# Kernel optimization log

Measured on AMD Instinct MI355X. Metric: run time of the kernel, lower is better.

The kernel has to match this reference:

```python
import jax, jax.numpy as jnp
import numpy as np

OUT_F, IN_F = 4096, 4096
NNZ = 838860
TOKENS = (8, 2048)


def setup_inputs() -> dict:
    key = jax.random.key(0)
    k1, k2, k3, k4, k5 = jax.random.split(key, 5)
    inp = {
        "input": jax.random.normal(k1, (*TOKENS, IN_F), dtype=jnp.float32),
        "dense_weights": jax.random.normal(k2, (OUT_F, IN_F), dtype=jnp.float32) * 0.02,
        "dense_bias": jax.random.normal(k3, (OUT_F,), dtype=jnp.float32) * 0.02,
        "sparse_weights": jax.random.normal(k4, (NNZ,), dtype=jnp.float32) * 0.02,
        "nz_idx": jnp.sort(jax.random.randint(k5, (NNZ,), 0, OUT_F * IN_F, dtype=jnp.int32)),
    }
    return inp


def reference(input, dense_weights, dense_bias, sparse_weights, nz_idx):
    # csr_add: scatter sparse delta into dense weight (CSR expressed as sorted flat indices)
    out_f, in_f = dense_weights.shape
    rows = nz_idx // in_f
    cols = nz_idx % in_f
    weights = dense_weights.at[rows, cols].add(sparse_weights)  # [out_f, in_f]
    # F.linear: x @ W.T + b
    return jnp.einsum('bsi,oi->bso', input, weights) + dense_bias
```

## Files before the change

### kernel.cpp

```cpp
#include <hip/hip_runtime.h>

typedef __bf16 bf16x8 __attribute__((ext_vector_type(8)));
typedef float  f32x4  __attribute__((ext_vector_type(4)));

#define IN_F  4096
#define OUT_F 4096
#define BM 256
#define BN 256
#define BK 32
#define NBUF 4
#define TILE_ELEMS (BM * BK)

__device__ inline unsigned int pk_bf16(float a, float b) {
  unsigned int ua = __float_as_uint(a);
  unsigned int ub = __float_as_uint(b);
  ua = (ua + 0x7FFFu + ((ua >> 16) & 1u)) >> 16;
  ub = (ub + 0x7FFFu + ((ub >> 16) & 1u)) >> 16;
  return ua | (ub << 16);
}
__device__ inline unsigned short bf16_1(float a) {
  unsigned int u = __float_as_uint(a);
  return (unsigned short)((u + 0x7FFFu + ((u >> 16) & 1u)) >> 16);
}

__global__ void cvt_f32_bf16_x8(const float4* __restrict__ src, uint4* __restrict__ dst, int n8) {
  int i = blockIdx.x * 256 + threadIdx.x;
  if (i >= n8) return;
  float4 a = src[2 * i];
  float4 b = src[2 * i + 1];
  uint4 o;
  o.x = pk_bf16(a.x, a.y);
  o.y = pk_bf16(a.z, a.w);
  o.z = pk_bf16(b.x, b.y);
  o.w = pk_bf16(b.z, b.w);
  dst[i] = o;
}

__global__ void sparse_fix_k(const float* __restrict__ dw, const int* __restrict__ idx,
                             const float* __restrict__ sv, unsigned short* __restrict__ wb,
                             int nnz) {
  int i = blockIdx.x * 256 + threadIdx.x;
  if (i >= nnz) return;
  int id = idx[i];
  if (i > 0 && idx[i - 1] == id) return;
  float s = sv[i];
  int j = i + 1;
  while (j < nnz && idx[j] == id) { s += sv[j]; ++j; }
  wb[id] = bf16_1(dw[id] + s);
}

__global__ __launch_bounds__(512, 2) void gemm256(
    const unsigned short* __restrict__ Xb,
    const unsigned short* __restrict__ Wb,
    const float* __restrict__ bias,
    float* __restrict__ out,
    int M, int N, int K)
{
  __shared__ __align__(16) unsigned short lA[NBUF * TILE_ELEMS];
  __shared__ __align__(16) unsigned short lB[NBUF * TILE_ELEMS];

  const int t    = threadIdx.x;
  const int w    = t >> 6;
  const int lane = t & 63;
  const int quad = lane >> 4;
  const int l16  = lane & 15;
  const int wr   = w >> 2;
  const int wc   = w & 3;

  const int nwg = gridDim.x;
  const int cpx = nwg >> 3;
  const int sid = (blockIdx.x & 7) * cpx + (blockIdx.x >> 3);
  const int gn  = N / BN;
  const int tile_n = (sid % gn) * BN;
  const int tile_m = (sid / gn) * BM;

  const int c0 = t, c1 = 512 + t;
  const int r0 = c0 >> 2, r1 = c1 >> 2;
  const int s0 = ((c0 & 3) ^ ((r0 >> 1) & 3)) * 8;
  const int s1 = ((c1 & 3) ^ ((r1 >> 1) & 3)) * 8;
  const unsigned short* aS0 = Xb + (size_t)(tile_m + r0) * K + s0;
  const unsigned short* aS1 = Xb + (size_t)(tile_m + r1) * K + s1;
  const unsigned short* bS0 = Wb + (size_t)(tile_n + r0) * K + s0;
  const unsigned short* bS1 = Wb + (size_t)(tile_n + r1) * K + s1;

#define GLD(src, dst) __builtin_amdgcn_global_load_lds( \
      (const __attribute__((address_space(1))) unsigned int*)(src), \
      (__attribute__((address_space(3))) unsigned int*)(dst), 16, 0, 0)
#define STAGE_A(tt) do { const int _b = ((tt) & 3) * TILE_ELEMS; const int _kb = (tt) * BK; \
      GLD(aS0 + _kb, lA + _b + c0 * 8); GLD(aS1 + _kb, lA + _b + c1 * 8); } while (0)
#define STAGE_B(tt) do { const int _b = ((tt) & 3) * TILE_ELEMS; const int _kb = (tt) * BK; \
      GLD(bS0 + _kb, lB + _b + c0 * 8); GLD(bS1 + _kb, lB + _b + c1 * 8); } while (0)

  int offA[8], offB[4];
#pragma unroll
  for (int mi = 0; mi < 8; ++mi) {
    const int ra = wr * 128 + mi * 16 + l16;
    offA[mi] = ra * BK + (quad ^ ((ra >> 1) & 3)) * 8;
  }
#pragma unroll
  for (int ni = 0; ni < 4; ++ni) {
    const int rb = wc * 64 + ni * 16 + l16;
    offB[ni] = rb * BK + (quad ^ ((rb >> 1) & 3)) * 8;
  }

  f32x4 acc[8][4] = {};
  const int nt = K / BK;

  STAGE_A(0); STAGE_B(0);
  STAGE_A(1); STAGE_B(1);
  STAGE_A(2); STAGE_B(2);
  asm volatile("s_waitcnt vmcnt(8)" ::: "memory");
  __builtin_amdgcn_s_barrier();

  for (int tt = 0; tt < nt; ++tt) {
    const unsigned short* bufA = lA + (tt & 3) * TILE_ELEMS;
    const unsigned short* bufB = lB + (tt & 3) * TILE_ELEMS;

    bf16x8 af0[4], bfr[4];
#pragma unroll
    for (int mi = 0; mi < 4; ++mi) af0[mi] = *(const bf16x8*)&bufA[offA[mi]];
#pragma unroll
    for (int ni = 0; ni < 4; ++ni) bfr[ni] = *(const bf16x8*)&bufB[offB[ni]];
    if (tt + 3 < nt) STAGE_A(tt + 3);
    __builtin_amdgcn_s_barrier();
    __builtin_amdgcn_s_setprio(1);
#pragma unroll
    for (int mi = 0; mi < 4; ++mi)
#pragma unroll
      for (int ni = 0; ni < 4; ++ni)
        acc[mi][ni] = __builtin_amdgcn_mfma_f32_16x16x32_bf16(af0[mi], bfr[ni], acc[mi][ni], 0, 0, 0);
    __builtin_amdgcn_s_setprio(0);
    __builtin_amdgcn_s_barrier();

    bf16x8 af1[4];
#pragma unroll
    for (int mi = 0; mi < 4; ++mi) af1[mi] = *(const bf16x8*)&bufA[offA[4 + mi]];
    if (tt + 3 < nt) STAGE_B(tt + 3);
    if (tt < nt - 3)       asm volatile("s_waitcnt vmcnt(8)" ::: "memory");
    else if (tt == nt - 3) asm volatile("s_waitcnt vmcnt(4)" ::: "memory");
    else if (tt == nt - 2) asm volatile("s_waitcnt vmcnt(0)" ::: "memory");
    __builtin_amdgcn_s_barrier();
    __builtin_amdgcn_s_setprio(1);
#pragma unroll
    for (int mi = 0; mi < 4; ++mi)
#pragma unroll
      for (int ni = 0; ni < 4; ++ni)
        acc[4 + mi][ni] = __builtin_amdgcn_mfma_f32_16x16x32_bf16(af1[mi], bfr[ni], acc[4 + mi][ni], 0, 0, 0);
    __builtin_amdgcn_s_setprio(0);
    __builtin_amdgcn_s_barrier();
  }

#pragma unroll
  for (int ni = 0; ni < 4; ++ni) {
    const int n = tile_n + wc * 64 + ni * 16 + l16;
    const float bv = bias[n];
#pragma unroll
    for (int mi = 0; mi < 8; ++mi) {
      const int m0 = tile_m + wr * 128 + mi * 16 + quad * 4;
#pragma unroll
      for (int r = 0; r < 4; ++r)
        out[(size_t)(m0 + r) * N + n] = acc[mi][ni][r] + bv;
    }
  }
#undef GLD
#undef STAGE_A
#undef STAGE_B
}

extern "C" void kernel_launch(void* const* d_in, const int* in_sizes, int n_in,
                              void* d_out, int out_size, void* d_ws, size_t ws_size,
                              hipStream_t stream) {
  const float* x    = (const float*)d_in[0];
  const float* dw   = (const float*)d_in[1];
  const float* bias = (const float*)d_in[2];
  const float* sv   = (const float*)d_in[3];
  const int*   idx  = (const int*)d_in[4];
  float* out = (float*)d_out;

  const int K = IN_F, N = OUT_F;
  const int M   = in_sizes[0] / K;
  const int nnz = in_sizes[3];
  const int WN  = N * K;

  unsigned short* ws_xb = (unsigned short*)d_ws;
  unsigned short* ws_wb = (unsigned short*)((char*)d_ws + (size_t)in_sizes[0] * 2);

  cvt_f32_bf16_x8<<<WN / 8 / 256, 256, 0, stream>>>((const float4*)dw, (uint4*)ws_wb, WN / 8);
  sparse_fix_k<<<(nnz + 255) / 256, 256, 0, stream>>>(dw, idx, sv, ws_wb, nnz);
  const int xn = in_sizes[0];
  cvt_f32_bf16_x8<<<xn / 8 / 256, 256, 0, stream>>>((const float4*)x, (uint4*)ws_xb, xn / 8);
  const int nblocks = (M / BM) * (N / BN);
  gemm256<<<nblocks, 512, 0, stream>>>(ws_xb, ws_wb, bias, out, M, N, K);
}
```

Before: 1.067 ms.

## Restructure GEMM mainloop to BK=64 double-buffered half-tile staging pipeline

Replaces the 4-buffer BK=32 ring with two BK=64 buffers, each split into two 32-wide halves. Every iteration now runs four MFMA phases, and the global-to-LDS loads for the next halves are staged between phases, with a separate peeled epilogue for the last tile. The aim is fewer loop iterations and finer-grained overlap of loads with compute while keeping the same LDS footprint. The wait and barrier counts are hand-tuned, so an ordering mistake could cause stalls or races.

```diff
diff --git a/kernel.cpp b/kernel.cpp
--- a/kernel.cpp
+++ b/kernel.cpp
@@ -7,8 +7,8 @@
 #define OUT_F 4096
 #define BM 256
 #define BN 256
-#define BK 32
-#define NBUF 4
+#define BK 64
+#define HALF_ELEMS (BM * 32)
 #define TILE_ELEMS (BM * BK)
 
 __device__ inline unsigned int pk_bf16(float a, float b) {
@@ -56,8 +56,8 @@
     float* __restrict__ out,
     int M, int N, int K)
 {
-  __shared__ __align__(16) unsigned short lA[NBUF * TILE_ELEMS];
-  __shared__ __align__(16) unsigned short lB[NBUF * TILE_ELEMS];
+  __shared__ __align__(16) unsigned short lA[2 * TILE_ELEMS];
+  __shared__ __align__(16) unsigned short lB[2 * TILE_ELEMS];
 
   const int t    = threadIdx.x;
   const int w    = t >> 6;
@@ -78,76 +78,143 @@
   const int r0 = c0 >> 2, r1 = c1 >> 2;
   const int s0 = ((c0 & 3) ^ ((r0 >> 1) & 3)) * 8;
   const int s1 = ((c1 & 3) ^ ((r1 >> 1) & 3)) * 8;
-  const unsigned short* aS0 = Xb + (size_t)(tile_m + r0) * K + s0;
-  const unsigned short* aS1 = Xb + (size_t)(tile_m + r1) * K + s1;
-  const unsigned short* bS0 = Wb + (size_t)(tile_n + r0) * K + s0;
-  const unsigned short* bS1 = Wb + (size_t)(tile_n + r1) * K + s1;
+  const unsigned short* AS0 = Xb + (size_t)(tile_m + r0) * K + s0;
+  const unsigned short* AS1 = Xb + (size_t)(tile_m + r1) * K + s1;
+  const unsigned short* BS0 = Wb + (size_t)(tile_n + r0) * K + s0;
+  const unsigned short* BS1 = Wb + (size_t)(tile_n + r1) * K + s1;
 
 #define GLD(src, dst) __builtin_amdgcn_global_load_lds( \
       (const __attribute__((address_space(1))) unsigned int*)(src), \
       (__attribute__((address_space(3))) unsigned int*)(dst), 16, 0, 0)
-#define STAGE_A(tt) do { const int _b = ((tt) & 3) * TILE_ELEMS; const int _kb = (tt) * BK; \
-      GLD(aS0 + _kb, lA + _b + c0 * 8); GLD(aS1 + _kb, lA + _b + c1 * 8); } while (0)
-#define STAGE_B(tt) do { const int _b = ((tt) & 3) * TILE_ELEMS; const int _kb = (tt) * BK; \
-      GLD(bS0 + _kb, lB + _b + c0 * 8); GLD(bS1 + _kb, lB + _b + c1 * 8); } while (0)
+#define STAGE(MAT, TT, H) do { \
+      const int _b = (((TT) & 1) << 14) + ((H) << 13); \
+      const int _k = ((TT) << 6) + ((H) << 5); \
+      GLD(MAT##S0 + _k, l##MAT + _b + c0 * 8); \
+      GLD(MAT##S1 + _k, l##MAT + _b + c1 * 8); } while (0)
+#define WAITV(n) asm volatile("s_waitcnt vmcnt(" #n ")" ::: "memory")
+#define BAR() __builtin_amdgcn_s_barrier()
 
   int offA[8], offB[4];
 #pragma unroll
   for (int mi = 0; mi < 8; ++mi) {
     const int ra = wr * 128 + mi * 16 + l16;
-    offA[mi] = ra * BK + (quad ^ ((ra >> 1) & 3)) * 8;
+    offA[mi] = ra * 32 + (quad ^ ((ra >> 1) & 3)) * 8;
   }
 #pragma unroll
   for (int ni = 0; ni < 4; ++ni) {
     const int rb = wc * 64 + ni * 16 + l16;
-    offB[ni] = rb * BK + (quad ^ ((rb >> 1) & 3)) * 8;
+    offB[ni] = rb * 32 + (quad ^ ((rb >> 1) & 3)) * 8;
   }
 
   f32x4 acc[8][4] = {};
-  const int nt = K / BK;
-
-  STAGE_A(0); STAGE_B(0);
-  STAGE_A(1); STAGE_B(1);
-  STAGE_A(2); STAGE_B(2);
-  asm volatile("s_waitcnt vmcnt(8)" ::: "memory");
-  __builtin_amdgcn_s_barrier();
-
-  for (int tt = 0; tt < nt; ++tt) {
-    const unsigned short* bufA = lA + (tt & 3) * TILE_ELEMS;
-    const unsigned short* bufB = lB + (tt & 3) * TILE_ELEMS;
-
-    bf16x8 af0[4], bfr[4];
-#pragma unroll
-    for (int mi = 0; mi < 4; ++mi) af0[mi] = *(const bf16x8*)&bufA[offA[mi]];
-#pragma unroll
-    for (int ni = 0; ni < 4; ++ni) bfr[ni] = *(const bf16x8*)&bufB[offB[ni]];
-    if (tt + 3 < nt) STAGE_A(tt + 3);
-    __builtin_amdgcn_s_barrier();
-    __builtin_amdgcn_s_setprio(1);
-#pragma unroll
-    for (int mi = 0; mi < 4; ++mi)
-#pragma unroll
-      for (int ni = 0; ni < 4; ++ni)
-        acc[mi][ni] = __builtin_amdgcn_mfma_f32_16x16x32_bf16(af0[mi], bfr[ni], acc[mi][ni], 0, 0, 0);
-    __builtin_amdgcn_s_setprio(0);
-    __builtin_amdgcn_s_barrier();
-
-    bf16x8 af1[4];
-#pragma unroll
-    for (int mi = 0; mi < 4; ++mi) af1[mi] = *(const bf16x8*)&bufA[offA[4 + mi]];
-    if (tt + 3 < nt) STAGE_B(tt + 3);
-    if (tt < nt - 3)       asm volatile("s_waitcnt vmcnt(8)" ::: "memory");
-    else if (tt == nt - 3) asm volatile("s_waitcnt vmcnt(4)" ::: "memory");
-    else if (tt == nt - 2) asm volatile("s_waitcnt vmcnt(0)" ::: "memory");
-    __builtin_amdgcn_s_barrier();
-    __builtin_amdgcn_s_setprio(1);
-#pragma unroll
-    for (int mi = 0; mi < 4; ++mi)
-#pragma unroll
-      for (int ni = 0; ni < 4; ++ni)
-        acc[4 + mi][ni] = __builtin_amdgcn_mfma_f32_16x16x32_bf16(af1[mi], bfr[ni], acc[4 + mi][ni], 0, 0, 0);
-    __builtin_amdgcn_s_setprio(0);
-    __builtin_amdgcn_s_barrier();
+  bf16x8 a0[4], a1[4], b0[4], b1[4];
+  const int NT = K / BK;
+
+  STAGE(A, 0, 0); STAGE(B, 0, 0);
+  STAGE(A, 0, 1); STAGE(B, 0, 1);
+  STAGE(A, 1, 0); STAGE(B, 1, 0);
+  WAITV(8);
+  BAR();
+
+  for (int T = 0; T < NT - 1; ++T) {
+    const unsigned short* bufA = lA + ((T & 1) << 14);
+    const unsigned short* bufB = lB + ((T & 1) << 14);
+    const bool st2 = (T + 2 < NT);
+
+#pragma unroll
+    for (int i = 0; i < 4; ++i) a0[i] = *(const bf16x8*)&bufA[offA[i]];
+#pragma unroll
+    for (int j = 0; j < 4; ++j) b0[j] = *(const bf16x8*)&bufB[offB[j]];
+    STAGE(A, T + 1, 1);
+    WAITV(8); BAR();
+    __builtin_amdgcn_s_setprio(1);
+#pragma unroll
+    for (int i = 0; i < 4; ++i)
+#pragma unroll
+      for (int j = 0; j < 4; ++j)
+        acc[i][j] = __builtin_amdgcn_mfma_f32_16x16x32_bf16(a0[i], b0[j], acc[i][j], 0, 0, 0);
+    __builtin_amdgcn_s_setprio(0);
+    BAR();
+
+#pragma unroll
+    for (int i = 0; i < 4; ++i) a1[i] = *(const bf16x8*)&bufA[offA[4 + i]];
+    STAGE(B, T + 1, 1);
+    WAITV(8); BAR();
+    __builtin_amdgcn_s_setprio(1);
+#pragma unroll
+    for (int i = 0; i < 4; ++i)
+#pragma unroll
+      for (int j = 0; j < 4; ++j)
+        acc[4 + i][j] = __builtin_amdgcn_mfma_f32_16x16x32_bf16(a1[i], b0[j], acc[4 + i][j], 0, 0, 0);
+    __builtin_amdgcn_s_setprio(0);
+    BAR();
+
+#pragma unroll
+    for (int i = 0; i < 4; ++i) a0[i] = *(const bf16x8*)&bufA[HALF_ELEMS + offA[i]];
+#pragma unroll
+    for (int j = 0; j < 4; ++j) b1[j] = *(const bf16x8*)&bufB[HALF_ELEMS + offB[j]];
+    if (st2) STAGE(A, T + 2, 0);
+    WAITV(8); BAR();
+    __builtin_amdgcn_s_setprio(1);
+#pragma unroll
+    for (int i = 0; i < 4; ++i)
+#pragma unroll
+      for (int j = 0; j < 4; ++j)
+        acc[i][j] = __builtin_amdgcn_mfma_f32_16x16x32_bf16(a0[i], b1[j], acc[i][j], 0, 0, 0);
+    __builtin_amdgcn_s_setprio(0);
+    BAR();
+
+#pragma unroll
+    for (int i = 0; i < 4; ++i) a1[i] = *(const bf16x8*)&bufA[HALF_ELEMS + offA[4 + i]];
+    if (st2) STAGE(B, T + 2, 0);
+    WAITV(8); BAR();
+    __builtin_amdgcn_s_setprio(1);
+#pragma unroll
+    for (int i = 0; i < 4; ++i)
+#pragma unroll
+      for (int j = 0; j < 4; ++j)
+        acc[4 + i][j] = __builtin_amdgcn_mfma_f32_16x16x32_bf16(a1[i], b1[j], acc[4 + i][j], 0, 0, 0);
+    __builtin_amdgcn_s_setprio(0);
+    BAR();
+  }
+
+  {
+    const int T = NT - 1;
+    WAITV(0); BAR();
+    const unsigned short* bufA = lA + ((T & 1) << 14);
+    const unsigned short* bufB = lB + ((T & 1) << 14);
+#pragma unroll
+    for (int i = 0; i < 4; ++i) a0[i] = *(const bf16x8*)&bufA[offA[i]];
+#pragma unroll
+    for (int j = 0; j < 4; ++j) b0[j] = *(const bf16x8*)&bufB[offB[j]];
+#pragma unroll
+    for (int i = 0; i < 4; ++i)
+#pragma unroll
+      for (int j = 0; j < 4; ++j)
+        acc[i][j] = __builtin_amdgcn_mfma_f32_16x16x32_bf16(a0[i], b0[j], acc[i][j], 0, 0, 0);
+#pragma unroll
+    for (int i = 0; i < 4; ++i) a1[i] = *(const bf16x8*)&bufA[offA[4 + i]];
+#pragma unroll
+    for (int i = 0; i < 4; ++i)
+#pragma unroll
+      for (int j = 0; j < 4; ++j)
+        acc[4 + i][j] = __builtin_amdgcn_mfma_f32_16x16x32_bf16(a1[i], b0[j], acc[4 + i][j], 0, 0, 0);
+#pragma unroll
+    for (int i = 0; i < 4; ++i) a0[i] = *(const bf16x8*)&bufA[HALF_ELEMS + offA[i]];
+#pragma unroll
+    for (int j = 0; j < 4; ++j) b1[j] = *(const bf16x8*)&bufB[HALF_ELEMS + offB[j]];
+#pragma unroll
+    for (int i = 0; i < 4; ++i)
+#pragma unroll
+      for (int j = 0; j < 4; ++j)
+        acc[i][j] = __builtin_amdgcn_mfma_f32_16x16x32_bf16(a0[i], b1[j], acc[i][j], 0, 0, 0);
+#pragma unroll
+    for (int i = 0; i < 4; ++i) a1[i] = *(const bf16x8*)&bufA[HALF_ELEMS + offA[4 + i]];
+#pragma unroll
+    for (int i = 0; i < 4; ++i)
+#pragma unroll
+      for (int j = 0; j < 4; ++j)
+        acc[4 + i][j] = __builtin_amdgcn_mfma_f32_16x16x32_bf16(a1[i], b1[j], acc[4 + i][j], 0, 0, 0);
   }
 
 #pragma unroll
@@ -163,8 +230,9 @@
     }
   }
 #undef GLD
-#undef STAGE_A
-#undef STAGE_B
+#undef STAGE
+#undef WAITV
+#undef BAR
 }
 
 extern "C" void kernel_launch(void* const* d_in, const int* in_sizes, int n_in,
```

New measurement: 1.059 ms. No clear change (-0.8%).

## Restructure GEMM pipeline to BK=64 double-buffer with half-tile staging

Applied to the files above, without the earlier changes.

Replaces the 4-deep BK=32 LDS ring with a 2-buffer BK=64 layout split into two 32-wide halves. Each K-tile is processed in four MFMA phases, with the next half-tiles prefetched between phases, unrolled by two tiles, plus an explicit drained epilogue. The aim is to cut loop overhead and per-iteration barrier and wait cost while keeping the same LDS footprint. The trade-off is more complex vmcnt accounting, which risks correctness or stalls if the wait counts are wrong.

```diff
diff --git a/kernel.cpp b/kernel.cpp
--- a/kernel.cpp
+++ b/kernel.cpp
@@ -7,8 +7,8 @@
 #define OUT_F 4096
 #define BM 256
 #define BN 256
-#define BK 32
-#define NBUF 4
+#define BK 64
+#define HALF_ELEMS (BM * 32)
 #define TILE_ELEMS (BM * BK)
 
 __device__ inline unsigned int pk_bf16(float a, float b) {
@@ -56,8 +56,8 @@
     float* __restrict__ out,
     int M, int N, int K)
 {
-  __shared__ __align__(16) unsigned short lA[NBUF * TILE_ELEMS];
-  __shared__ __align__(16) unsigned short lB[NBUF * TILE_ELEMS];
+  __shared__ __align__(16) unsigned short lA[2 * TILE_ELEMS];
+  __shared__ __align__(16) unsigned short lB[2 * TILE_ELEMS];
 
   const int t    = threadIdx.x;
   const int w    = t >> 6;
@@ -78,77 +78,89 @@
   const int r0 = c0 >> 2, r1 = c1 >> 2;
   const int s0 = ((c0 & 3) ^ ((r0 >> 1) & 3)) * 8;
   const int s1 = ((c1 & 3) ^ ((r1 >> 1) & 3)) * 8;
-  const unsigned short* aS0 = Xb + (size_t)(tile_m + r0) * K + s0;
-  const unsigned short* aS1 = Xb + (size_t)(tile_m + r1) * K + s1;
-  const unsigned short* bS0 = Wb + (size_t)(tile_n + r0) * K + s0;
-  const unsigned short* bS1 = Wb + (size_t)(tile_n + r1) * K + s1;
+  const unsigned short* AS0 = Xb + (size_t)(tile_m + r0) * K + s0;
+  const unsigned short* AS1 = Xb + (size_t)(tile_m + r1) * K + s1;
+  const unsigned short* BS0 = Wb + (size_t)(tile_n + r0) * K + s0;
+  const unsigned short* BS1 = Wb + (size_t)(tile_n + r1) * K + s1;
 
 #define GLD(src, dst) __builtin_amdgcn_global_load_lds( \
       (const __attribute__((address_space(1))) unsigned int*)(src), \
       (__attribute__((address_space(3))) unsigned int*)(dst), 16, 0, 0)
-#define STAGE_A(tt) do { const int _b = ((tt) & 3) * TILE_ELEMS; const int _kb = (tt) * BK; \
-      GLD(aS0 + _kb, lA + _b + c0 * 8); GLD(aS1 + _kb, lA + _b + c1 * 8); } while (0)
-#define STAGE_B(tt) do { const int _b = ((tt) & 3) * TILE_ELEMS; const int _kb = (tt) * BK; \
-      GLD(bS0 + _kb, lB + _b + c0 * 8); GLD(bS1 + _kb, lB + _b + c1 * 8); } while (0)
+#define STAGE(MAT, TT, H) do { \
+      const int _b = (((TT) & 1) << 14) + ((H) << 13); \
+      const int _k = ((TT) << 6) + ((H) << 5); \
+      GLD(MAT##S0 + _k, l##MAT + _b + c0 * 8); \
+      GLD(MAT##S1 + _k, l##MAT + _b + c1 * 8); } while (0)
+#define WAITV(n) asm volatile("s_waitcnt vmcnt(" #n ")" ::: "memory")
+#define BAR() __builtin_amdgcn_s_barrier()
 
   int offA[8], offB[4];
 #pragma unroll
   for (int mi = 0; mi < 8; ++mi) {
     const int ra = wr * 128 + mi * 16 + l16;
-    offA[mi] = ra * BK + (quad ^ ((ra >> 1) & 3)) * 8;
+    offA[mi] = ra * 32 + (quad ^ ((ra >> 1) & 3)) * 8;
   }
 #pragma unroll
   for (int ni = 0; ni < 4; ++ni) {
     const int rb = wc * 64 + ni * 16 + l16;
-    offB[ni] = rb * BK + (quad ^ ((rb >> 1) & 3)) * 8;
+    offB[ni] = rb * 32 + (quad ^ ((rb >> 1) & 3)) * 8;
   }
 
   f32x4 acc[8][4] = {};
-  const int nt = K / BK;
-
-  STAGE_A(0); STAGE_B(0);
-  STAGE_A(1); STAGE_B(1);
-  STAGE_A(2); STAGE_B(2);
-  asm volatile("s_waitcnt vmcnt(8)" ::: "memory");
-  __builtin_amdgcn_s_barrier();
-
-  for (int tt = 0; tt < nt; ++tt) {
-    const unsigned short* bufA = lA + (tt & 3) * TILE_ELEMS;
-    const unsigned short* bufB = lB + (tt & 3) * TILE_ELEMS;
-
-    bf16x8 af0[4], bfr[4];
-#pragma unroll
-    for (int mi = 0; mi < 4; ++mi) af0[mi] = *(const bf16x8*)&bufA[offA[mi]];
-#pragma unroll
-    for (int ni = 0; ni < 4; ++ni) bfr[ni] = *(const bf16x8*)&bufB[offB[ni]];
-    if (tt + 3 < nt) STAGE_A(tt + 3);
-    __builtin_amdgcn_s_barrier();
+  bf16x8 a0[4], a1[4], b0[4], b1[4];
+  const int NT = K / BK;
+
+  auto rd4 = [&](bf16x8* d, const unsigned short* base, const int* off) {
+#pragma unroll
+    for (int i = 0; i < 4; ++i) d[i] = *(const bf16x8*)&base[off[i]];
+  };
+  auto mf = [&](const int R, const bf16x8* at, const bf16x8* bt) {
     __builtin_amdgcn_s_setprio(1);
 #pragma unroll
-    for (int mi = 0; mi < 4; ++mi)
-#pragma unroll
-      for (int ni = 0; ni < 4; ++ni)
-        acc[mi][ni] = __builtin_amdgcn_mfma_f32_16x16x32_bf16(af0[mi], bfr[ni], acc[mi][ni], 0, 0, 0);
+    for (int i = 0; i < 4; ++i)
+#pragma unroll
+      for (int j = 0; j < 4; ++j)
+        acc[R + i][j] = __builtin_amdgcn_mfma_f32_16x16x32_bf16(at[i], bt[j], acc[R + i][j], 0, 0, 0);
     __builtin_amdgcn_s_setprio(0);
-    __builtin_amdgcn_s_barrier();
-
-    bf16x8 af1[4];
-#pragma unroll
-    for (int mi = 0; mi < 4; ++mi) af1[mi] = *(const bf16x8*)&bufA[offA[4 + mi]];
-    if (tt + 3 < nt) STAGE_B(tt + 3);
-    if (tt < nt - 3)       asm volatile("s_waitcnt vmcnt(8)" ::: "memory");
-    else if (tt == nt - 3) asm volatile("s_waitcnt vmcnt(4)" ::: "memory");
-    else if (tt == nt - 2) asm volatile("s_waitcnt vmcnt(0)" ::: "memory");
-    __builtin_amdgcn_s_barrier();
-    __builtin_amdgcn_s_setprio(1);
-#pragma unroll
-    for (int mi = 0; mi < 4; ++mi)
-#pragma unroll
-      for (int ni = 0; ni < 4; ++ni)
-        acc[4 + mi][ni] = __builtin_amdgcn_mfma_f32_16x16x32_bf16(af1[mi], bfr[ni], acc[4 + mi][ni], 0, 0, 0);
-    __builtin_amdgcn_s_setprio(0);
-    __builtin_amdgcn_s_barrier();
-  }
+  };
+
+#define TILE_PHASES(BB, TT)                                                   \
+    rd4(a0, lA + (BB), offA); rd4(b0, lB + (BB), offB);                       \
+    STAGE(A, (TT) + 1, 1);                                                    \
+    BAR(); mf(0, a0, b0); BAR();                                              \
+    rd4(a1, lA + (BB), offA + 4);                                             \
+    STAGE(B, (TT) + 1, 1);                                                    \
+    WAITV(8); BAR(); mf(4, a1, b0); BAR();                                    \
+    rd4(a0, lA + (BB) + HALF_ELEMS, offA); rd4(b1, lB + (BB) + HALF_ELEMS, offB); \
+    STAGE(A, (TT) + 2, 0);                                                    \
+    BAR(); mf(0, a0, b1); BAR();                                              \
+    rd4(a1, lA + (BB) + HALF_ELEMS, offA + 4);                                \
+    STAGE(B, (TT) + 2, 0);                                                    \
+    WAITV(8); BAR(); mf(4, a1, b1); BAR();
+
+#define TILE_DRAINED(BB)                                                      \
+    rd4(a0, lA + (BB), offA); rd4(b0, lB + (BB), offB);                       \
+    mf(0, a0, b0);                                                            \
+    rd4(a1, lA + (BB), offA + 4); mf(4, a1, b0);                              \
+    rd4(a0, lA + (BB) + HALF_ELEMS, offA); rd4(b1, lB + (BB) + HALF_ELEMS, offB); \
+    mf(0, a0, b1);                                                            \
+    rd4(a1, lA + (BB) + HALF_ELEMS, offA + 4); mf(4, a1, b1);
+
+  STAGE(A, 0, 0); STAGE(B, 0, 0);
+  STAGE(A, 0, 1); STAGE(B, 0, 1);
+  STAGE(A, 1, 0); STAGE(B, 1, 0);
+  WAITV(8);
+  BAR();
+
+  for (int T = 0; T < NT - 2; T += 2) {
+    TILE_PHASES(0, T)
+    TILE_PHASES(TILE_ELEMS, T + 1)
+  }
+
+  STAGE(A, NT - 1, 1); STAGE(B, NT - 1, 1);
+  WAITV(0); BAR();
+  TILE_DRAINED(0)
+  TILE_DRAINED(TILE_ELEMS)
 
 #pragma unroll
   for (int ni = 0; ni < 4; ++ni) {
@@ -163,8 +175,11 @@
     }
   }
 #undef GLD
-#undef STAGE_A
-#undef STAGE_B
+#undef STAGE
+#undef WAITV
+#undef BAR
+#undef TILE_PHASES
+#undef TILE_DRAINED
 }
 
 extern "C" void kernel_launch(void* const* d_in, const int* in_sizes, int n_in,
```

New measurement: 1.000 ms. 1.07x faster.
